# Performance work log

Hardware: AMD Instinct MI355X
Metric: run time of the kernel (lower is better)

Reference implementation:

```python
import jax, jax.numpy as jnp
import numpy as np

B, N, E = 2, 2048, 1024
H, D = 16, 64  # context_dim = H*D = 1024


def setup_inputs() -> dict:
    key = jax.random.key(0)
    ks = jax.random.split(key, 6)
    s = 0.02
    return {
        "input_emb": jax.random.normal(ks[0], (B, N, E), dtype=jnp.float32),
        "Wq": jax.random.normal(ks[1], (E, H * D), dtype=jnp.float32) * s,
        "Wk": jax.random.normal(ks[2], (E, D), dtype=jnp.float32) * s,
        "Wv": jax.random.normal(ks[3], (E, D), dtype=jnp.float32) * s,
        "Wo": jax.random.normal(ks[4], (H * D, H * D), dtype=jnp.float32) * s,
        "bo": jax.random.normal(ks[5], (H * D,), dtype=jnp.float32) * s,
    }


def reference(input_emb, Wq, Wk, Wv, Wo, bo):
    b, n, _ = input_emb.shape
    Q = (input_emb @ Wq).reshape(b, n, H, D)          # (B,N,H,D)
    K = input_emb @ Wk                                 # (B,N,D) shared across heads (MQA)
    V = input_emb @ Wv                                 # (B,N,D)
    # scores: (B,H,N,N); mask is applied before scaling in the torch code,
    # but -inf/scale == -inf so mask-then-scale == scale-then-mask.
    scores = jnp.einsum("bnhd,bmd->bhnm", Q, K) / jnp.sqrt(jnp.float32(D))
    causal = jnp.tril(jnp.ones((n, n), dtype=bool))    # True = keep
    scores = jnp.where(causal[None, None], scores, -jnp.inf)
    weights = jax.nn.softmax(scores, axis=-1)          # dropout rate 0.0 -> identity
    Z = jnp.einsum("bhnm,bmd->bnhd", weights, V).reshape(b, n, H * D)
    return Z @ Wo + bo
```

## Files before the change

### kernel.cpp

```cpp
#include <hip/hip_runtime.h>
#include <hip/hip_bf16.h>


#define NQ 2048
#define BATCH 2
#define HEADS 16
#define HD 64
#define EMB 1024
#define NKV 1152

typedef short s16x8 __attribute__((ext_vector_type(8)));
typedef float f32x4 __attribute__((ext_vector_type(4)));
typedef unsigned int u32x4 __attribute__((ext_vector_type(4)));
typedef unsigned short ushort_t;

__device__ __forceinline__ ushort_t f2bf(float f) {
    unsigned u = __builtin_bit_cast(unsigned, f);
    u += 0x7fff + ((u >> 16) & 1);
    return (ushort_t)(u >> 16);
}

__device__ __forceinline__ void store_out(float* p, float v) { *p = v; }
__device__ __forceinline__ void store_out(ushort_t* p, float v) { *p = f2bf(v); }

#define GL16(g, l)                                                                  \
    __builtin_amdgcn_global_load_lds(                                               \
        (const __attribute__((address_space(1))) unsigned int*)(g),                 \
        (__attribute__((address_space(3))) unsigned int*)(l), 16, 0, 0)

__global__ __launch_bounds__(256) void prep(const float* __restrict__ x,
                                            const float* __restrict__ Wq,
                                            const float* __restrict__ Wk,
                                            const float* __restrict__ Wv,
                                            const float* __restrict__ Wo,
                                            ushort_t* __restrict__ xb,
                                            ushort_t* __restrict__ Wqkv_t,
                                            ushort_t* __restrict__ Wo_t) {
    const int bid = blockIdx.x, t = threadIdx.x;
    if (bid < 4096) {
        const int i = bid * 1024 + t * 4;
        const float4 v = *(const float4*)&x[i];
        ushort_t o[4] = {f2bf(v.x), f2bf(v.y), f2bf(v.z), f2bf(v.w)};
        *(uint2*)&xb[i] = *(uint2*)o;
        return;
    }
    int tb = bid - 4096;
    const float* src; ushort_t* dst; int N, n0, k0;
    if (tb < 1024)      { src = Wq; N = 1024; dst = Wqkv_t;
                          n0 = (tb & 31) * 32; k0 = (tb >> 5) * 32; }
    else if (tb < 1088) { tb -= 1024; src = Wk; N = 64; dst = Wqkv_t + (size_t)1024 * EMB;
                          n0 = (tb & 1) * 32; k0 = (tb >> 1) * 32; }
    else if (tb < 1152) { tb -= 1088; src = Wv; N = 64; dst = Wqkv_t + (size_t)1088 * EMB;
                          n0 = (tb & 1) * 32; k0 = (tb >> 1) * 32; }
    else                { tb -= 1152; src = Wo; N = 1024; dst = Wo_t;
                          n0 = (tb & 31) * 32; k0 = (tb >> 5) * 32; }
    __shared__ float tile[32][33];
    const int tx = t & 31, ty = t >> 5;
#pragma unroll
    for (int i = 0; i < 32; i += 8)
        tile[ty + i][tx] = src[(size_t)(k0 + ty + i) * N + n0 + tx];
    __syncthreads();
#pragma unroll
    for (int i = 0; i < 32; i += 8)
        dst[(size_t)(n0 + ty + i) * EMB + k0 + tx] = f2bf(tile[tx][ty + i]);
}

__device__ __forceinline__ s16x8 frag(const ushort_t* lds, int row, int lc) {
    const int phys = lc ^ (row & 7);
    return *(const s16x8*)&lds[row * 64 + phys * 8];
}

template<bool HAS_BIAS, bool WRITE_VT, typename OutT>
__global__ __launch_bounds__(256, 2) void gemm_bf16(const ushort_t* __restrict__ A,
                                                    const ushort_t* __restrict__ Bt,
                                                    const float* __restrict__ bias,
                                                    OutT* __restrict__ C,
                                                    ushort_t* __restrict__ Vt,
                                                    int M, int N, int K) {
    __shared__ __align__(16) ushort_t Al[2][128 * 64];
    __shared__ __align__(16) ushort_t Bl[2][128 * 64];
    const int t = threadIdx.x;
    const int w = t >> 6, lane = t & 63, quad = lane >> 4, ln = lane & 15;
    const int wm = w >> 1, wn = w & 1;

    const int nwg = gridDim.x * gridDim.y;
    int lin = blockIdx.y * gridDim.x + blockIdx.x;
    lin = (lin & 7) * (nwg >> 3) + (lin >> 3);
    const int bx = lin % gridDim.x, by = lin / gridDim.x;
    const int row0 = by * 128, col0 = bx * 128;

    const ushort_t* pA[4];
    const ushort_t* pB[4];
#pragma unroll
    for (int it = 0; it < 4; ++it) {
        const int u = (w * 4 + it) * 64 + lane;
        const int row = u >> 3, pc = u & 7;
        const int lc = pc ^ (row & 7);
        pA[it] = A + (size_t)(row0 + row) * K + lc * 8;
        pB[it] = Bt + (size_t)(col0 + row) * K + lc * 8;
    }

#define STAGE_AB(la, lb)                                                            \
    {                                                                               \
        _Pragma("unroll")                                                           \
        for (int it = 0; it < 4; ++it) {                                            \
            GL16(pA[it], (la) + (w * 4 + it) * 512);                                \
            GL16(pB[it], (lb) + (w * 4 + it) * 512);                                \
            pA[it] += 64;                                                           \
            pB[it] += 64;                                                           \
        }                                                                           \
    }

    f32x4 acc[4][4] = {};
    const int nk = K >> 6;

    STAGE_AB(Al[0], Bl[0]);
    __syncthreads();

#pragma unroll 1
    for (int ks = 0; ks < nk; ++ks) {
        const int cur = ks & 1;
        if (ks + 1 < nk) STAGE_AB(Al[cur ^ 1], Bl[cur ^ 1]);

        const ushort_t* la = Al[cur];
        const ushort_t* lb = Bl[cur];
        s16x8 af[4][2], bf[4][2];
#pragma unroll
        for (int mt = 0; mt < 4; ++mt) {
            af[mt][0] = frag(la, wm * 64 + mt * 16 + ln, quad);
            af[mt][1] = frag(la, wm * 64 + mt * 16 + ln, 4 + quad);
        }
#pragma unroll
        for (int nt = 0; nt < 4; ++nt) {
            bf[nt][0] = frag(lb, wn * 64 + nt * 16 + ln, quad);
            bf[nt][1] = frag(lb, wn * 64 + nt * 16 + ln, 4 + quad);
        }
#pragma unroll
        for (int mt = 0; mt < 4; ++mt)
#pragma unroll
            for (int nt = 0; nt < 4; ++nt) {
                acc[mt][nt] = __builtin_amdgcn_mfma_f32_16x16x32_bf16(
                    af[mt][0], bf[nt][0], acc[mt][nt], 0, 0, 0);
                acc[mt][nt] = __builtin_amdgcn_mfma_f32_16x16x32_bf16(
                    af[mt][1], bf[nt][1], acc[mt][nt], 0, 0, 0);
            }
        __syncthreads();
    }
#undef STAGE_AB

#pragma unroll
    for (int nt = 0; nt < 4; ++nt) {
        const int col = col0 + wn * 64 + nt * 16 + ln;
        const float bv = HAS_BIAS ? bias[col] : 0.f;
#pragma unroll
        for (int mt = 0; mt < 4; ++mt) {
#pragma unroll
            for (int r = 0; r < 4; ++r) {
                const int row = row0 + wm * 64 + mt * 16 + quad * 4 + r;
                float v = acc[mt][nt][r] + bv;
                if (WRITE_VT && col < 1024) v *= 0.18033688011112043f;
                store_out(&C[(size_t)row * N + col], v);
            }
            if (WRITE_VT && col >= 1088) {
                const int d = col - 1088;
                const int n = row0 + wm * 64 + mt * 16 + quad * 4;
                const int bb = n >> 11, nn = n & 2047;
                ushort_t tmp[4] = {f2bf(acc[mt][nt][0]), f2bf(acc[mt][nt][1]),
                                   f2bf(acc[mt][nt][2]), f2bf(acc[mt][nt][3])};
                *(uint2*)&Vt[((size_t)bb * 64 + d) * NQ + nn] = *(uint2*)tmp;
            }
        }
    }
}

__device__ __forceinline__ void stage_tile(ushort_t* lds, const ushort_t* g,
                                           size_t rstride, int w, int lane) {
#pragma unroll
    for (int it = 0; it < 2; ++it) {
        const int u = (w * 2 + it) * 64 + lane;
        const int row = u >> 3, pc = u & 7;
        const int lc = pc ^ (row & 7);
        GL16(g + (size_t)row * rstride + lc * 8, lds + (size_t)(w * 2 + it) * 512);
    }
}

__device__ __forceinline__ void stage_k(ushort_t* lds, const ushort_t* g,
                                        int w, int lane) {
#pragma unroll
    for (int it = 0; it < 2; ++it) {
        const int u = (w * 2 + it) * 64 + lane;
        const int row = u >> 3, pc = u & 7;
        const int lc = pc ^ (row & 7);
        const int grow = (row & 32) | (((row >> 2) & 3) << 3) |
                         (((row >> 4) & 1) << 2) | (row & 3);
        GL16(g + (size_t)grow * NKV + lc * 8, lds + (size_t)(w * 2 + it) * 512);
    }
}

__global__ __launch_bounds__(256, 4) void attn_mfma(const ushort_t* __restrict__ QKV,
                                                    const ushort_t* __restrict__ Vt,
                                                    ushort_t* __restrict__ Z) {
    const int bid = blockIdx.x;
    const int b = (bid >> 4) & 1, h = bid & 15;
    const int i = bid >> 5, k = i >> 3, j = i & 7;
    const int qt = (k == 0) ? 2 * j : (k == 1) ? 31 - 2 * j
                 : (k == 2) ? 2 * j + 1 : 30 - 2 * j;
    const int t = threadIdx.x;
    const int w = t >> 6, lane = t & 63, quad = lane >> 4, ln = lane & 15;

    __shared__ __align__(16) ushort_t Kl[2][64 * 64];
    __shared__ __align__(16) ushort_t Vl[2][64 * 64];

    const ushort_t* Kg = QKV + (size_t)b * NQ * NKV + 1024;
    const ushort_t* Vg = Vt + (size_t)b * 64 * NQ;

    const ushort_t* Qg = QKV + (size_t)(b * NQ + qt * 64 + w * 16 + ln) * NKV + h * HD;
    const s16x8 aQ0 = *(const s16x8*)(Qg + quad * 8);
    const s16x8 aQ1 = *(const s16x8*)(Qg + 32 + quad * 8);

    stage_k(Kl[0], Kg, w, lane);
    stage_tile(Vl[0], Vg, NQ, w, lane);
    __syncthreads();

    f32x4 o[4];
#pragma unroll
    for (int ii = 0; ii < 4; ++ii) o[ii] = f32x4{0.f, 0.f, 0.f, 0.f};
    float mrow = -1e30f, lrow = 0.f;
    const int qrel = w * 16 + ln;

#pragma unroll 1
    for (int jt = 0; jt <= qt; ++jt) {
        const int cur = jt & 1;
        if (jt < qt) {
            stage_k(Kl[cur ^ 1], Kg + (size_t)(jt + 1) * 64 * NKV, w, lane);
            stage_tile(Vl[cur ^ 1], Vg + (jt + 1) * 64, NQ, w, lane);
        }
        const ushort_t* Kc = Kl[cur];
        const ushort_t* Vc = Vl[cur];

        f32x4 s[4];
        __builtin_amdgcn_s_setprio(1);
#pragma unroll
        for (int nt = 0; nt < 4; ++nt) {
            f32x4 acc = f32x4{0.f, 0.f, 0.f, 0.f};
            acc = __builtin_amdgcn_mfma_f32_16x16x32_bf16(
                frag(Kc, nt * 16 + ln, quad), aQ0, acc, 0, 0, 0);
            acc = __builtin_amdgcn_mfma_f32_16x16x32_bf16(
                frag(Kc, nt * 16 + ln, 4 + quad), aQ1, acc, 0, 0, 0);
            s[nt] = acc;
        }
        __builtin_amdgcn_s_setprio(0);

        if (jt == qt) {
#pragma unroll
            for (int nt = 0; nt < 4; ++nt)
#pragma unroll
                for (int r = 0; r < 4; ++r) {
                    const int kv = (nt >> 1) * 32 + quad * 8 + (nt & 1) * 4 + r;
                    if (kv > qrel) s[nt][r] = -1e30f;
                }
        }

        float m0 = fmaxf(fmaxf(s[0][0], s[0][1]), fmaxf(s[0][2], s[0][3]));
        float m1 = fmaxf(fmaxf(s[1][0], s[1][1]), fmaxf(s[1][2], s[1][3]));
        float m2 = fmaxf(fmaxf(s[2][0], s[2][1]), fmaxf(s[2][2], s[2][3]));
        float m3 = fmaxf(fmaxf(s[3][0], s[3][1]), fmaxf(s[3][2], s[3][3]));
        float rmax = fmaxf(fmaxf(m0, m1), fmaxf(m2, m3));
        rmax = fmaxf(rmax, __shfl_xor(rmax, 16));
        rmax = fmaxf(rmax, __shfl_xor(rmax, 32));

        if (!__all(rmax - mrow <= 8.f)) {
            const float mnew = fmaxf(mrow, rmax);
            const float al = __builtin_amdgcn_exp2f(mrow - mnew);
            mrow = mnew;
            lrow *= al;
#pragma unroll
            for (int ntd = 0; ntd < 4; ++ntd)
#pragma unroll
                for (int r = 0; r < 4; ++r) o[ntd][r] *= al;
        }

        float rsum = 0.f;
#pragma unroll
        for (int nt = 0; nt < 4; ++nt)
#pragma unroll
            for (int r = 0; r < 4; ++r) {
                const float pv = __builtin_amdgcn_exp2f(s[nt][r] - mrow);
                s[nt][r] = pv;
                rsum += pv;
            }
        rsum += __shfl_xor(rsum, 16);
        rsum += __shfl_xor(rsum, 32);
        lrow += rsum;

        unsigned pw0[4], pw1[4];
#pragma unroll
        for (int jj = 0; jj < 4; ++jj) {
            const int nt0 = jj >> 1, rr = 2 * (jj & 1);
            asm("v_cvt_pk_bf16_f32 %0, %1, %2"
                : "=v"(pw0[jj]) : "v"(s[nt0][rr]), "v"(s[nt0][rr + 1]));
            asm("v_cvt_pk_bf16_f32 %0, %1, %2"
                : "=v"(pw1[jj]) : "v"(s[2 + nt0][rr]), "v"(s[2 + nt0][rr + 1]));
        }
        const u32x4 q0 = {pw0[0], pw0[1], pw0[2], pw0[3]};
        const u32x4 q1 = {pw1[0], pw1[1], pw1[2], pw1[3]};
        const s16x8 bP0 = __builtin_bit_cast(s16x8, q0);
        const s16x8 bP1 = __builtin_bit_cast(s16x8, q1);

        __builtin_amdgcn_s_setprio(1);
#pragma unroll
        for (int ntd = 0; ntd < 4; ++ntd) {
            o[ntd] = __builtin_amdgcn_mfma_f32_16x16x32_bf16(
                frag(Vc, ntd * 16 + ln, quad), bP0, o[ntd], 0, 0, 0);
            o[ntd] = __builtin_amdgcn_mfma_f32_16x16x32_bf16(
                frag(Vc, ntd * 16 + ln, 4 + quad), bP1, o[ntd], 0, 0, 0);
        }
        __builtin_amdgcn_s_setprio(0);
        __syncthreads();
    }

    const float invl = 1.f / lrow;
    const size_t row = (size_t)(b * NQ + qt * 64 + w * 16 + ln);
#pragma unroll
    for (int ntd = 0; ntd < 4; ++ntd) {
        ushort_t tmp[4];
#pragma unroll
        for (int r = 0; r < 4; ++r) tmp[r] = f2bf(o[ntd][r] * invl);
        *(uint2*)&Z[row * EMB + h * HD + ntd * 16 + quad * 4] = *(uint2*)tmp;
    }
}

extern "C" void kernel_launch(void* const* d_in, const int* in_sizes, int n_in,
                              void* d_out, int out_size, void* d_ws, size_t ws_size,
                              hipStream_t stream) {
    const float* x  = (const float*)d_in[0];
    const float* Wq = (const float*)d_in[1];
    const float* Wk = (const float*)d_in[2];
    const float* Wv = (const float*)d_in[3];
    const float* Wo = (const float*)d_in[4];
    const float* bo = (const float*)d_in[5];
    float* out = (float*)d_out;

    const int M = BATCH * NQ;
    char* ws = (char*)d_ws;
    ushort_t* xb     = (ushort_t*)ws;
    ushort_t* Wqkv_t = (ushort_t*)(ws + (size_t)8  * 1024 * 1024);
    ushort_t* Wo_t   = (ushort_t*)(ws + (size_t)11 * 1024 * 1024);
    ushort_t* QKV    = (ushort_t*)(ws + (size_t)13 * 1024 * 1024);
    ushort_t* Vt     = (ushort_t*)(ws + (size_t)23 * 1024 * 1024);
    ushort_t* Zb     = (ushort_t*)(ws + (size_t)24 * 1024 * 1024);

    dim3 blk(256);
    prep<<<dim3(6272), blk, 0, stream>>>(x, Wq, Wk, Wv, Wo, xb, Wqkv_t, Wo_t);
    gemm_bf16<false, true, ushort_t><<<dim3(NKV / 128, M / 64 / 2), blk, 0, stream>>>(
        xb, Wqkv_t, nullptr, QKV, Vt, M, NKV, EMB);
    attn_mfma<<<dim3(1024), blk, 0, stream>>>(QKV, Vt, Zb);
    gemm_bf16<true, false, float><<<dim3(EMB / 128, M / 64 / 2), blk, 0, stream>>>(
        Zb, Wo_t, bo, out, nullptr, M, EMB, EMB);
}
```

Before: 161.1 us.

## Share K/V tiles across four heads per block in MQA attention

Each attention block now covers four heads, one per wave, and 32 query rows split into two 16-row sub-tiles per wave, instead of one head and 64 rows. Because K and V are shared across heads (MQA), each staged LDS K/V tile is reused by four heads, cutting global and LDS staging traffic per unit of work. K/V fragments are read once per tile and reused across both query sub-tiles, and the query-tile order is remapped to balance causal work. The costs are higher register pressure (launch bounds lowered to 2 blocks per SIMD), half as many blocks, and a finer 32-row causal granularity.

Result: slower. 170.2 us (+5.6%).

```diff
diff --git a/kernel.cpp b/kernel.cpp
--- a/kernel.cpp
+++ b/kernel.cpp
@@ -197,16 +197,21 @@
     }
 }
 
-__global__ __launch_bounds__(256, 4) void attn_mfma(const ushort_t* __restrict__ QKV,
+__global__ __launch_bounds__(256, 2) void attn_mfma(const ushort_t* __restrict__ QKV,
                                                     const ushort_t* __restrict__ Vt,
                                                     ushort_t* __restrict__ Z) {
     const int bid = blockIdx.x;
-    const int b = (bid >> 4) & 1, h = bid & 15;
-    const int i = bid >> 5, k = i >> 3, j = i & 7;
-    const int qt = (k == 0) ? 2 * j : (k == 1) ? 31 - 2 * j
-                 : (k == 2) ? 2 * j + 1 : 30 - 2 * j;
+    const int g = bid & 7, u = bid >> 3;
+    const int hg = u & 3, tt = u >> 2;
+    const int ib = g + 8 * tt;
+    const int b = ib & 1, iq = ib >> 1;
+    const int m = (iq < 32) ? iq : 95 - iq;
+    const int iters = (m >> 1) + 1;
+    const int qbase = m * 32;
+
     const int t = threadIdx.x;
     const int w = t >> 6, lane = t & 63, quad = lane >> 4, ln = lane & 15;
+    const int h = hg * 4 + w;
 
     __shared__ __align__(16) ushort_t Kl[2][64 * 64];
     __shared__ __align__(16) ushort_t Vl[2][64 * 64];
@@ -214,119 +219,161 @@
     const ushort_t* Kg = QKV + (size_t)b * NQ * NKV + 1024;
     const ushort_t* Vg = Vt + (size_t)b * 64 * NQ;
 
-    const ushort_t* Qg = QKV + (size_t)(b * NQ + qt * 64 + w * 16 + ln) * NKV + h * HD;
-    const s16x8 aQ0 = *(const s16x8*)(Qg + quad * 8);
-    const s16x8 aQ1 = *(const s16x8*)(Qg + 32 + quad * 8);
+    s16x8 aQ[2][2];
+#pragma unroll
+    for (int ss = 0; ss < 2; ++ss) {
+        const ushort_t* Qg =
+            QKV + (size_t)(b * NQ + qbase + ss * 16 + ln) * NKV + h * HD;
+        aQ[ss][0] = *(const s16x8*)(Qg + quad * 8);
+        aQ[ss][1] = *(const s16x8*)(Qg + 32 + quad * 8);
+    }
 
     stage_k(Kl[0], Kg, w, lane);
     stage_tile(Vl[0], Vg, NQ, w, lane);
     __syncthreads();
 
-    f32x4 o[4];
-#pragma unroll
-    for (int ii = 0; ii < 4; ++ii) o[ii] = f32x4{0.f, 0.f, 0.f, 0.f};
-    float mrow = -1e30f, lrow = 0.f;
-    const int qrel = w * 16 + ln;
+    f32x4 o[2][4];
+#pragma unroll
+    for (int ss = 0; ss < 2; ++ss)
+#pragma unroll
+        for (int ii = 0; ii < 4; ++ii) o[ss][ii] = f32x4{0.f, 0.f, 0.f, 0.f};
+    float mrow[2] = {-1e30f, -1e30f}, lrow[2] = {0.f, 0.f};
 
 #pragma unroll 1
-    for (int jt = 0; jt <= qt; ++jt) {
+    for (int jt = 0; jt < iters; ++jt) {
         const int cur = jt & 1;
-        if (jt < qt) {
+        if (jt + 1 < iters) {
             stage_k(Kl[cur ^ 1], Kg + (size_t)(jt + 1) * 64 * NKV, w, lane);
             stage_tile(Vl[cur ^ 1], Vg + (jt + 1) * 64, NQ, w, lane);
         }
         const ushort_t* Kc = Kl[cur];
         const ushort_t* Vc = Vl[cur];
 
-        f32x4 s[4];
+        s16x8 kf0[4], kf1[4];
+#pragma unroll
+        for (int nt = 0; nt < 4; ++nt) {
+            kf0[nt] = frag(Kc, nt * 16 + ln, quad);
+            kf1[nt] = frag(Kc, nt * 16 + ln, 4 + quad);
+        }
+
+        f32x4 sx[2][4];
         __builtin_amdgcn_s_setprio(1);
 #pragma unroll
+        for (int ss = 0; ss < 2; ++ss)
+#pragma unroll
+            for (int nt = 0; nt < 4; ++nt) {
+                f32x4 acc = f32x4{0.f, 0.f, 0.f, 0.f};
+                acc = __builtin_amdgcn_mfma_f32_16x16x32_bf16(kf0[nt], aQ[ss][0],
+                                                              acc, 0, 0, 0);
+                acc = __builtin_amdgcn_mfma_f32_16x16x32_bf16(kf1[nt], aQ[ss][1],
+                                                              acc, 0, 0, 0);
+                sx[ss][nt] = acc;
+            }
+        __builtin_amdgcn_s_setprio(0);
+
+        s16x8 vf0[4], vf1[4];
+#pragma unroll
         for (int nt = 0; nt < 4; ++nt) {
-            f32x4 acc = f32x4{0.f, 0.f, 0.f, 0.f};
-            acc = __builtin_amdgcn_mfma_f32_16x16x32_bf16(
-                frag(Kc, nt * 16 + ln, quad), aQ0, acc, 0, 0, 0);
-            acc = __builtin_amdgcn_mfma_f32_16x16x32_bf16(
-                frag(Kc, nt * 16 + ln, 4 + quad), aQ1, acc, 0, 0, 0);
-            s[nt] = acc;
-        }
-        __builtin_amdgcn_s_setprio(0);
-
-        if (jt == qt) {
+            vf0[nt] = frag(Vc, nt * 16 + ln, quad);
+            vf1[nt] = frag(Vc, nt * 16 + ln, 4 + quad);
+        }
+
+        if (jt == iters - 1) {
+#pragma unroll
+            for (int ss = 0; ss < 2; ++ss) {
+                const int qa = qbase + ss * 16 + ln;
+#pragma unroll
+                for (int nt = 0; nt < 4; ++nt)
+#pragma unroll
+                    for (int r = 0; r < 4; ++r) {
+                        const int kv =
+                            jt * 64 + (nt >> 1) * 32 + quad * 8 + (nt & 1) * 4 + r;
+                        if (kv > qa) sx[ss][nt][r] = -1e30f;
+                    }
+            }
+        }
+
+        unsigned bp0[2][4], bp1[2][4];
+#pragma unroll
+        for (int ss = 0; ss < 2; ++ss) {
+            const float r0 = fmaxf(fmaxf(sx[ss][0][0], sx[ss][0][1]),
+                                   fmaxf(sx[ss][0][2], sx[ss][0][3]));
+            const float r1 = fmaxf(fmaxf(sx[ss][1][0], sx[ss][1][1]),
+                                   fmaxf(sx[ss][1][2], sx[ss][1][3]));
+            const float r2 = fmaxf(fmaxf(sx[ss][2][0], sx[ss][2][1]),
+                                   fmaxf(sx[ss][2][2], sx[ss][2][3]));
+            const float r3 = fmaxf(fmaxf(sx[ss][3][0], sx[ss][3][1]),
+                                   fmaxf(sx[ss][3][2], sx[ss][3][3]));
+            float rmax = fmaxf(fmaxf(r0, r1), fmaxf(r2, r3));
+            rmax = fmaxf(rmax, __shfl_xor(rmax, 16));
+            rmax = fmaxf(rmax, __shfl_xor(rmax, 32));
+
+            if (!__all(rmax - mrow[ss] <= 8.f)) {
+                const float mnew = fmaxf(mrow[ss], rmax);
+                const float al = __builtin_amdgcn_exp2f(mrow[ss] - mnew);
+                mrow[ss] = mnew;
+                lrow[ss] *= al;
+#pragma unroll
+                for (int ntd = 0; ntd < 4; ++ntd)
+#pragma unroll
+                    for (int r = 0; r < 4; ++r) o[ss][ntd][r] *= al;
+            }
+
+            float rsum = 0.f;
 #pragma unroll
             for (int nt = 0; nt < 4; ++nt)
 #pragma unroll
                 for (int r = 0; r < 4; ++r) {
-                    const int kv = (nt >> 1) * 32 + quad * 8 + (nt & 1) * 4 + r;
-                    if (kv > qrel) s[nt][r] = -1e30f;
+                    const float pv = __builtin_amdgcn_exp2f(sx[ss][nt][r] - mrow[ss]);
+                    sx[ss][nt][r] = pv;
+                    rsum += pv;
                 }
-        }
-
-        float m0 = fmaxf(fmaxf(s[0][0], s[0][1]), fmaxf(s[0][2], s[0][3]));
-        float m1 = fmaxf(fmaxf(s[1][0], s[1][1]), fmaxf(s[1][2], s[1][3]));
-        float m2 = fmaxf(fmaxf(s[2][0], s[2][1]), fmaxf(s[2][2], s[2][3]));
-        float m3 = fmaxf(fmaxf(s[3][0], s[3][1]), fmaxf(s[3][2], s[3][3]));
-        float rmax = fmaxf(fmaxf(m0, m1), fmaxf(m2, m3));
-        rmax = fmaxf(rmax, __shfl_xor(rmax, 16));
-        rmax = fmaxf(rmax, __shfl_xor(rmax, 32));
-
-        if (!__all(rmax - mrow <= 8.f)) {
-            const float mnew = fmaxf(mrow, rmax);
-            const float al = __builtin_amdgcn_exp2f(mrow - mnew);
-            mrow = mnew;
-            lrow *= al;
-#pragma unroll
-            for (int ntd = 0; ntd < 4; ++ntd)
-#pragma unroll
-                for (int r = 0; r < 4; ++r) o[ntd][r] *= al;
-        }
-
-        float rsum = 0.f;
-#pragma unroll
-        for (int nt = 0; nt < 4; ++nt)
-#pragma unroll
-            for (int r = 0; r < 4; ++r) {
-                const float pv = __builtin_amdgcn_exp2f(s[nt][r] - mrow);
-                s[nt][r] = pv;
-                rsum += pv;
-            }
-        rsum += __shfl_xor(rsum, 16);
-        rsum += __shfl_xor(rsum, 32);
-        lrow += rsum;
-
-        unsigned pw0[4], pw1[4];
-#pragma unroll
-        for (int jj = 0; jj < 4; ++jj) {
-            const int nt0 = jj >> 1, rr = 2 * (jj & 1);
-            asm("v_cvt_pk_bf16_f32 %0, %1, %2"
-                : "=v"(pw0[jj]) : "v"(s[nt0][rr]), "v"(s[nt0][rr + 1]));
-            asm("v_cvt_pk_bf16_f32 %0, %1, %2"
-                : "=v"(pw1[jj]) : "v"(s[2 + nt0][rr]), "v"(s[2 + nt0][rr + 1]));
-        }
-        const u32x4 q0 = {pw0[0], pw0[1], pw0[2], pw0[3]};
-        const u32x4 q1 = {pw1[0], pw1[1], pw1[2], pw1[3]};
-        const s16x8 bP0 = __builtin_bit_cast(s16x8, q0);
-        const s16x8 bP1 = __builtin_bit_cast(s16x8, q1);
+            rsum += __shfl_xor(rsum, 16);
+            rsum += __shfl_xor(rsum, 32);
+            lrow[ss] += rsum;
+
+#pragma unroll
+            for (int jj = 0; jj < 4; ++jj) {
+                const int nt0 = jj >> 1, rr = 2 * (jj & 1);
+                asm("v_cvt_pk_bf16_f32 %0, %1, %2"
+                    : "=v"(bp0[ss][jj])
+                    : "v"(sx[ss][nt0][rr]), "v"(sx[ss][nt0][rr + 1]));
+                asm("v_cvt_pk_bf16_f32 %0, %1, %2"
+                    : "=v"(bp1[ss][jj])
+                    : "v"(sx[ss][2 + nt0][rr]), "v"(sx[ss][2 + nt0][rr + 1]));
+            }
+        }
 
         __builtin_amdgcn_s_setprio(1);
 #pragma unroll
-        for (int ntd = 0; ntd < 4; ++ntd) {
-            o[ntd] = __builtin_amdgcn_mfma_f32_16x16x32_bf16(
-                frag(Vc, ntd * 16 + ln, quad), bP0, o[ntd], 0, 0, 0);
-            o[ntd] = __builtin_amdgcn_mfma_f32_16x16x32_bf16(
-                frag(Vc, ntd * 16 + ln, 4 + quad), bP1, o[ntd], 0, 0, 0);
+        for (int ss = 0; ss < 2; ++ss) {
+            const s16x8 bP0 = __builtin_bit_cast(
+                s16x8, u32x4{bp0[ss][0], bp0[ss][1], bp0[ss][2], bp0[ss][3]});
+            const s16x8 bP1 = __builtin_bit_cast(
+                s16x8, u32x4{bp1[ss][0], bp1[ss][1], bp1[ss][2], bp1[ss][3]});
+#pragma unroll
+            for (int ntd = 0; ntd < 4; ++ntd) {
+                o[ss][ntd] = __builtin_amdgcn_mfma_f32_16x16x32_bf16(
+                    vf0[ntd], bP0, o[ss][ntd], 0, 0, 0);
+                o[ss][ntd] = __builtin_amdgcn_mfma_f32_16x16x32_bf16(
+                    vf1[ntd], bP1, o[ss][ntd], 0, 0, 0);
+            }
         }
         __builtin_amdgcn_s_setprio(0);
         __syncthreads();
     }
 
-    const float invl = 1.f / lrow;
-    const size_t row = (size_t)(b * NQ + qt * 64 + w * 16 + ln);
-#pragma unroll
-    for (int ntd = 0; ntd < 4; ++ntd) {
-        ushort_t tmp[4];
-#pragma unroll
-        for (int r = 0; r < 4; ++r) tmp[r] = f2bf(o[ntd][r] * invl);
-        *(uint2*)&Z[row * EMB + h * HD + ntd * 16 + quad * 4] = *(uint2*)tmp;
+#pragma unroll
+    for (int ss = 0; ss < 2; ++ss) {
+        const float invl = 1.f / lrow[ss];
+        const size_t row = (size_t)(b * NQ + qbase + ss * 16 + ln);
+#pragma unroll
+        for (int ntd = 0; ntd < 4; ++ntd) {
+            ushort_t tmp[4];
+#pragma unroll
+            for (int r = 0; r < 4; ++r) tmp[r] = f2bf(o[ss][ntd][r] * invl);
+            *(uint2*)&Z[row * EMB + h * HD + ntd * 16 + quad * 4] = *(uint2*)tmp;
+        }
     }
 }
 
@@ -354,7 +401,7 @@
     prep<<<dim3(6272), blk, 0, stream>>>(x, Wq, Wk, Wv, Wo, xb, Wqkv_t, Wo_t);
     gemm_bf16<false, true, ushort_t><<<dim3(NKV / 128, M / 64 / 2), blk, 0, stream>>>(
         xb, Wqkv_t, nullptr, QKV, Vt, M, NKV, EMB);
-    attn_mfma<<<dim3(1024), blk, 0, stream>>>(QKV, Vt, Zb);
+    attn_mfma<<<dim3(512), blk, 0, stream>>>(QKV, Vt, Zb);
     gemm_bf16<true, false, float><<<dim3(EMB / 128, M / 64 / 2), blk, 0, stream>>>(
         Zb, Wo_t, bo, out, nullptr, M, EMB, EMB);
 }
```
